# Kernel tuning notes

Measured on AMD Instinct MI355X. Metric: run time of the kernel, lower is better.

Reference implementation:

```python
import jax, jax.numpy as jnp
import numpy as np

N_NODES = 20000
N_EDGES = 500000
D_IN = 256
D_HID = 256
NUM_REL = 5
LL_OUT = 16
METAPATHS = [[0, 1], [2, 3]]  # relation id per hop, per metapath
N_CONVS = sum(len(mp) for mp in METAPATHS)  # 4 (all 256->256 since D_IN==D_HID)


def setup_inputs() -> dict:
    key = jax.random.key(0)
    ks = jax.random.split(key, 12)
    x = jax.random.normal(ks[0], (N_NODES, D_IN), dtype=jnp.float32)
    edge_index = jax.random.randint(ks[1], (2, N_EDGES), 0, N_NODES)
    edge_type = jax.random.randint(ks[2], (N_EDGES,), 0, NUM_REL)
    s = 1.0 / np.sqrt(D_HID)
    rel_W = jax.random.normal(ks[3], (N_CONVS, NUM_REL, D_HID, D_HID), dtype=jnp.float32) * s
    root_W = jax.random.normal(ks[4], (N_CONVS, D_HID, D_HID), dtype=jnp.float32) * s
    bias = jax.random.normal(ks[5], (N_CONVS, D_HID), dtype=jnp.float32) * s
    fc1_w = jax.random.normal(ks[6], (D_HID * len(METAPATHS), D_HID), dtype=jnp.float32) * s
    fc1_b = jnp.zeros((D_HID,), dtype=jnp.float32)
    fc2_w = jax.random.normal(ks[7], (D_HID, LL_OUT), dtype=jnp.float32) * s
    fc2_b = jnp.zeros((LL_OUT,), dtype=jnp.float32)
    return {"x": x, "edge_index": edge_index, "edge_type": edge_type,
            "rel_W": rel_W, "root_W": root_W, "bias": bias,
            "fc1_w": fc1_w, "fc1_b": fc1_b, "fc2_w": fc2_w, "fc2_b": fc2_b}


def _rgcn_conv(rel, h, W, R, b, src, dst, edge_type, n_nodes):
    # single-relation RGCN hop, flow='target_to_source': src node i aggregates
    # transformed features of its dst neighbors over edges with type==rel (mean).
    m = (edge_type == rel).astype(h.dtype)              # [E]
    hr = h @ W[rel]                                     # [N, D]
    msg = hr[dst] * m[:, None]                          # [E, D]
    agg = jax.ops.segment_sum(msg, src, num_segments=n_nodes)
    cnt = jax.ops.segment_sum(m, src, num_segments=n_nodes)
    agg = agg / jnp.maximum(cnt, 1.0)[:, None]
    return agg + h @ R + b


def reference(x, edge_index, edge_type, rel_W, root_W, bias, fc1_w, fc1_b, fc2_w, fc2_b):
    src, dst = edge_index[0], edge_index[1]
    n = x.shape[0]
    embs = []
    ci = 0
    for mp in METAPATHS:
        h = x
        for rel in mp:
            h = jax.nn.relu(_rgcn_conv(rel, h, rel_W[ci], root_W[ci], bias[ci],
                                       src, dst, edge_type, n))
            ci += 1
        embs.append(h)
    hcat = jnp.concatenate(embs, axis=1)                # [N, D_HID*n_metapaths]
    h = jax.nn.relu(hcat @ fc1_w + fc1_b)
    h = h @ fc2_w + fc2_b
    return jax.nn.log_softmax(h, axis=1)
```

## Files before the change

kernel.cpp:

```cpp
#include <hip/hip_runtime.h>
#include <hip/hip_bf16.h>

#define D 256
typedef unsigned short u16;
typedef __attribute__((ext_vector_type(8))) short bf16x8;
typedef __attribute__((ext_vector_type(4))) float f32x4;

__device__ inline u16 f2bf(float f) {
    unsigned u = __builtin_bit_cast(unsigned, f);
    unsigned r = (u + 0x7fff + ((u >> 16) & 1)) >> 16;
    return (u16)r;
}
__device__ inline float bf2f(u16 u) {
    return __builtin_bit_cast(float, (unsigned)u << 16);
}


__global__ void hist_kernel(const int* __restrict__ src, const int* __restrict__ et,
                            int* __restrict__ cnt, int E, int N) {
    int e = blockIdx.x * blockDim.x + threadIdx.x;
    if (e < E) {
        int r = et[e];
        if (r < 4) atomicAdd(&cnt[r * N + src[e]], 1);
    }
}

#define SCAN_BLK 4096

__global__ __launch_bounds__(256) void scan_reduce_kernel(const int* __restrict__ cnt,
        int* __restrict__ bsum, int n) {
    __shared__ int s[256];
    int base = blockIdx.x * SCAN_BLK;
    int t = threadIdx.x;
    int sum = 0;
    for (int i = t; i < SCAN_BLK; i += 256) {
        int idx = base + i;
        if (idx < n) sum += cnt[idx];
    }
    s[t] = sum;
    __syncthreads();
    for (int off = 128; off > 0; off >>= 1) {
        if (t < off) s[t] += s[t + off];
        __syncthreads();
    }
    if (t == 0) bsum[blockIdx.x] = s[0];
}

__global__ __launch_bounds__(256) void scan_sums_kernel(const int* __restrict__ bsum,
        int* __restrict__ boff, int nb, int* __restrict__ row_ptr, int n) {
    __shared__ int s[256];
    int t = threadIdx.x;
    s[t] = (t < nb) ? bsum[t] : 0;
    __syncthreads();
    for (int off = 1; off < 256; off <<= 1) {
        int v = (t >= off) ? s[t - off] : 0;
        __syncthreads();
        s[t] += v;
        __syncthreads();
    }
    if (t < nb) boff[t] = (t == 0) ? 0 : s[t - 1];
    if (t == 255) row_ptr[n] = s[255];
}

__global__ __launch_bounds__(256) void scan_out_kernel(const int* __restrict__ cnt,
        const int* __restrict__ boff, int* __restrict__ row_ptr,
        int* __restrict__ row_cur, int n) {
    __shared__ int stage[SCAN_BLK];
    __shared__ int part[256];
    int base = blockIdx.x * SCAN_BLK;
    int t = threadIdx.x;
    for (int i = t; i < SCAN_BLK; i += 256) {
        int idx = base + i;
        stage[i] = (idx < n) ? cnt[idx] : 0;
    }
    __syncthreads();
    int loc = 0;
#pragma unroll
    for (int j = 0; j < 16; ++j) loc += stage[t * 16 + j];
    part[t] = loc;
    __syncthreads();
    for (int off = 1; off < 256; off <<= 1) {
        int v = (t >= off) ? part[t - off] : 0;
        __syncthreads();
        part[t] += v;
        __syncthreads();
    }
    int run = boff[blockIdx.x] + ((t == 0) ? 0 : part[t - 1]);
#pragma unroll
    for (int j = 0; j < 16; ++j) {
        int idx = base + t * 16 + j;
        if (idx < n) {
            row_ptr[idx] = run;
            row_cur[idx] = run;
        }
        run += stage[t * 16 + j];
    }
}

__global__ void scatter_kernel(const int* __restrict__ src, const int* __restrict__ dst,
        const int* __restrict__ et, int* __restrict__ row_cur, int* __restrict__ eperm,
        int E, int N) {
    int e = blockIdx.x * blockDim.x + threadIdx.x;
    if (e < E) {
        int r = et[e];
        if (r < 4) {
            int pos = atomicAdd(&row_cur[r * N + src[e]], 1);
            eperm[pos] = dst[e];
        }
    }
}


__global__ void cast_x_kernel(const float* __restrict__ x, u16* __restrict__ xb, int n4) {
    int i = blockIdx.x * blockDim.x + threadIdx.x;
    if (i < n4) {
        float4 v = reinterpret_cast<const float4*>(x)[i];
        ushort4 o;
        o.x = f2bf(v.x); o.y = f2bf(v.y); o.z = f2bf(v.z); o.w = f2bf(v.w);
        reinterpret_cast<ushort4*>(xb)[i] = o;
    }
}

__global__ void build_wt_kernel(const float* __restrict__ rel_W,
                                const float* __restrict__ root_W, u16* __restrict__ Wcat) {
    int t = blockIdx.x * blockDim.x + threadIdx.x;
    int k = t & 255;
    int n = (t >> 8) & 511;
    int ci = t >> 17;
    float v;
    if (n < 256) v = rel_W[(((size_t)ci * 5 + ci) * 256 + k) * 256 + n];
    else         v = root_W[((size_t)ci * 256 + k) * 256 + (n - 256)];
    Wcat[t] = f2bf(v);
}

__global__ void build_fc1t_kernel(const float* __restrict__ fc1_w, u16* __restrict__ fc1t) {
    int t = blockIdx.x * blockDim.x + threadIdx.x;
    int k = t & 511;
    int n = t >> 9;
    fc1t[t] = f2bf(fc1_w[(size_t)k * 256 + n]);
}

__global__ void build_fc2t_kernel(const float* __restrict__ fc2_w, u16* __restrict__ fc2t) {
    int t = blockIdx.x * blockDim.x + threadIdx.x;
    int k = t & 255;
    int col = t >> 8;
    fc2t[t] = f2bf(fc2_w[(size_t)k * 16 + col]);
}


#define BM 64
#define BN 128
#define BK 64

template <int MODE>
__global__ __launch_bounds__(256) void gemm_mfma(
        const u16* __restrict__ A, const u16* __restrict__ Bt, int M, int K,
        u16* __restrict__ out_bf, u16* __restrict__ out_root,
        const float* __restrict__ bias, int ldo_bf) {
    __shared__ u16 Bs[BN * BK];

    const int tid  = threadIdx.x;
    const int wave = tid >> 6, lane = tid & 63;
    const int l15 = lane & 15, lg = lane >> 4;
    const int m0 = blockIdx.x * BM + wave * 16;
    const int n0 = blockIdx.y * BN;

    f32x4 acc[8];
#pragma unroll
    for (int j = 0; j < 8; ++j) acc[j] = (f32x4){0.f, 0.f, 0.f, 0.f};

    const int  arow = m0 + l15;
    const bool aval = arow < M;
    const u16* Arow = A + (size_t)arow * K;

    for (int k0 = 0; k0 < K; k0 += BK) {
        __syncthreads();
#pragma unroll
        for (int i = 0; i < 4; ++i) {
            int phys = i * 4096 + tid * 16;
            int n    = phys >> 7;
            int cl   = (phys & 127) ^ ((n & 7) << 4);
            const u16* srcp = Bt + (size_t)(n0 + n) * K + k0 + (cl >> 1);
            __builtin_amdgcn_global_load_lds(
                (const __attribute__((address_space(1))) void*)srcp,
                (__attribute__((address_space(3))) void*)((char*)Bs + phys), 16, 0, 0);
        }
        bf16x8 afr[2];
        if (aval) {
            afr[0] = *reinterpret_cast<const bf16x8*>(Arow + k0 + lg * 8);
            afr[1] = *reinterpret_cast<const bf16x8*>(Arow + k0 + 32 + lg * 8);
        } else {
            afr[0] = afr[1] = (bf16x8){0, 0, 0, 0, 0, 0, 0, 0};
        }
        __syncthreads();
#pragma unroll
        for (int kk = 0; kk < 2; ++kk) {
#pragma unroll
            for (int j = 0; j < 8; ++j) {
                int n    = j * 16 + l15;
                int cl   = kk * 64 + lg * 16;
                int phys = n * 128 + (cl ^ ((n & 7) << 4));
                bf16x8 bfr = *reinterpret_cast<const bf16x8*>((const char*)Bs + phys);
                acc[j] = __builtin_amdgcn_mfma_f32_16x16x32_bf16(afr[kk], bfr, acc[j], 0, 0, 0);
            }
        }
    }

    const int orow = m0 + lg * 4;
#pragma unroll
    for (int j = 0; j < 8; ++j) {
        int gn = n0 + j * 16 + l15;
#pragma unroll
        for (int r = 0; r < 4; ++r) {
            int m = orow + r;
            if (m >= M) continue;
            float v = acc[j][r];
            if (MODE == 0) {
                if (gn < 256) out_bf[(size_t)m * 256 + gn] = f2bf(v);
                else          out_root[(size_t)m * 256 + gn - 256] = f2bf(v + bias[gn - 256]);
            } else {
                v = fmaxf(v + bias[gn], 0.0f);
                out_bf[(size_t)m * ldo_bf + gn] = f2bf(v);
            }
        }
    }
}


__global__ __launch_bounds__(256) void aggregate_kernel(const u16* __restrict__ hr,
        const int* __restrict__ row_ptr, const int* __restrict__ eperm,
        const u16* __restrict__ rootb, u16* __restrict__ dst,
        int ldo, int coff, int N) {
    int node = blockIdx.x * 4 + (threadIdx.x >> 6);
    int lane = threadIdx.x & 63;
    if (node >= N) return;

    int beg = row_ptr[node];
    int end = row_ptr[node + 1];
    float a0 = 0.f, a1 = 0.f, a2 = 0.f, a3 = 0.f;
    for (int e = beg; e < end; ++e) {
        int d = eperm[e];
        ushort4 v = *reinterpret_cast<const ushort4*>(hr + (size_t)d * 256 + lane * 4);
        a0 += bf2f(v.x); a1 += bf2f(v.y); a2 += bf2f(v.z); a3 += bf2f(v.w);
    }
    float inv = 1.0f / fmaxf((float)(end - beg), 1.0f);
    ushort4 r4 = *reinterpret_cast<const ushort4*>(rootb + (size_t)node * 256 + lane * 4);
    ushort4 o;
    o.x = f2bf(fmaxf(fmaf(a0, inv, bf2f(r4.x)), 0.0f));
    o.y = f2bf(fmaxf(fmaf(a1, inv, bf2f(r4.y)), 0.0f));
    o.z = f2bf(fmaxf(fmaf(a2, inv, bf2f(r4.z)), 0.0f));
    o.w = f2bf(fmaxf(fmaf(a3, inv, bf2f(r4.w)), 0.0f));
    *reinterpret_cast<ushort4*>(dst + (size_t)node * ldo + coff + lane * 4) = o;
}


__global__ __launch_bounds__(256) void head_mfma_kernel(const u16* __restrict__ hid,
        const u16* __restrict__ w2t, const float* __restrict__ b2,
        float* __restrict__ out, int N) {
    int tile = blockIdx.x * 4 + (threadIdx.x >> 6);
    int lane = threadIdx.x & 63;
    int l15 = lane & 15, lg = lane >> 4;
    int ntiles = (N + 15) / 16;
    if (tile >= ntiles) return;

    int anode = tile * 16 + l15;
    if (anode >= N) anode = N - 1;
    const u16* Arow = hid + (size_t)anode * 256;
    const u16* Brow = w2t + (size_t)l15 * 256;

    f32x4 acc = (f32x4){0.f, 0.f, 0.f, 0.f};
#pragma unroll
    for (int k0 = 0; k0 < 256; k0 += 32) {
        bf16x8 a = *reinterpret_cast<const bf16x8*>(Arow + k0 + lg * 8);
        bf16x8 b = *reinterpret_cast<const bf16x8*>(Brow + k0 + lg * 8);
        acc = __builtin_amdgcn_mfma_f32_16x16x32_bf16(a, b, acc, 0, 0, 0);
    }
    float bcol = b2[l15];
#pragma unroll
    for (int r = 0; r < 4; ++r) {
        float v = acc[r] + bcol;
        float mx = v;
        mx = fmaxf(mx, __shfl_xor(mx, 1));
        mx = fmaxf(mx, __shfl_xor(mx, 2));
        mx = fmaxf(mx, __shfl_xor(mx, 4));
        mx = fmaxf(mx, __shfl_xor(mx, 8));
        float e = expf(v - mx);
        float s = e;
        s += __shfl_xor(s, 1);
        s += __shfl_xor(s, 2);
        s += __shfl_xor(s, 4);
        s += __shfl_xor(s, 8);
        float lse = mx + logf(s);
        int row = tile * 16 + lg * 4 + r;
        if (row < N) out[(size_t)row * 16 + l15] = v - lse;
    }
}


extern "C" void kernel_launch(void* const* d_in, const int* in_sizes, int n_in,
                              void* d_out, int out_size, void* d_ws, size_t ws_size,
                              hipStream_t stream) {
    const float* x      = (const float*)d_in[0];
    const int*   ei     = (const int*)d_in[1];
    const int*   et     = (const int*)d_in[2];
    const float* rel_W  = (const float*)d_in[3];
    const float* root_W = (const float*)d_in[4];
    const float* bias   = (const float*)d_in[5];
    const float* fc1_w  = (const float*)d_in[6];
    const float* fc1_b  = (const float*)d_in[7];
    const float* fc2_w  = (const float*)d_in[8];
    const float* fc2_b  = (const float*)d_in[9];
    float* out = (float*)d_out;

    const int N = in_sizes[0] / D;
    const int E = in_sizes[2];
    const int* src = ei;
    const int* dst = ei + E;

    char* w = (char*)d_ws;
    u16* xb    = (u16*)w;  w += (size_t)N * 256 * 2;
    u16* h1b   = (u16*)w;  w += (size_t)N * 256 * 2;
    u16* hcatb = (u16*)w;  w += (size_t)N * 512 * 2;
    u16* hr    = (u16*)w;  w += (size_t)N * 256 * 2;
    u16* rootb = (u16*)w;  w += (size_t)N * 256 * 2;
    u16* Wcat  = (u16*)w;  w += (size_t)4 * 512 * 256 * 2;
    u16* fc1t  = (u16*)w;  w += (size_t)256 * 512 * 2;
    u16* fc2t  = (u16*)w;  w += (size_t)16 * 256 * 2;
    int* cnt     = (int*)w;  w += (size_t)4 * N * 4;
    int* row_ptr = (int*)w;  w += ((size_t)4 * N + 1) * 4;
    int* row_cur = (int*)w;  w += (size_t)4 * N * 4;
    int* eperm   = (int*)w;  w += (size_t)E * 4;
    int* bsum    = (int*)w;  w += 256 * 4;
    int* boff    = (int*)w;  w += 256 * 4;
    u16* hid = h1b;

    const int n_keys = 4 * N;
    const int nb = (n_keys + SCAN_BLK - 1) / SCAN_BLK;

    hipMemsetAsync(cnt, 0, (size_t)n_keys * 4, stream);
    hist_kernel<<<dim3((E + 255) / 256), dim3(256), 0, stream>>>(src, et, cnt, E, N);
    scan_reduce_kernel<<<dim3(nb), dim3(256), 0, stream>>>(cnt, bsum, n_keys);
    scan_sums_kernel<<<dim3(1), dim3(256), 0, stream>>>(bsum, boff, nb, row_ptr, n_keys);
    scan_out_kernel<<<dim3(nb), dim3(256), 0, stream>>>(cnt, boff, row_ptr, row_cur, n_keys);
    scatter_kernel<<<dim3((E + 255) / 256), dim3(256), 0, stream>>>(src, dst, et, row_cur, eperm, E, N);

    cast_x_kernel<<<dim3((N * 256 / 4 + 255) / 256), dim3(256), 0, stream>>>(x, xb, N * 256 / 4);
    build_wt_kernel<<<dim3(4 * 512 * 256 / 256), dim3(256), 0, stream>>>(rel_W, root_W, Wcat);
    build_fc1t_kernel<<<dim3(256 * 512 / 256), dim3(256), 0, stream>>>(fc1_w, fc1t);
    build_fc2t_kernel<<<dim3(16), dim3(256), 0, stream>>>(fc2_w, fc2t);

    dim3 gblock(256);
    dim3 ngrid((N + 3) / 4);
    dim3 cgrid((N + BM - 1) / BM, 512 / BN);
    dim3 fgrid((N + BM - 1) / BM, 256 / BN);

    for (int ci = 0; ci < 4; ++ci) {
        int mp = ci >> 1, hop = ci & 1;
        const u16* hin = (hop == 0) ? xb : h1b;
        gemm_mfma<0><<<cgrid, gblock, 0, stream>>>(hin, Wcat + (size_t)ci * 512 * 256,
                N, 256, hr, rootb, bias + (size_t)ci * 256, 256);
        u16* dstb; int ldo, coff;
        if (hop == 0) { dstb = h1b;   ldo = 256; coff = 0; }
        else          { dstb = hcatb; ldo = 512; coff = mp * 256; }
        aggregate_kernel<<<ngrid, gblock, 0, stream>>>(hr, row_ptr + (size_t)ci * N, eperm,
                rootb, dstb, ldo, coff, N);
    }
    gemm_mfma<1><<<fgrid, gblock, 0, stream>>>(hcatb, fc1t, N, 512, hid, nullptr, fc1_b, 256);
    int ntiles = (N + 15) / 16;
    head_mfma_kernel<<<dim3((ntiles + 3) / 4), gblock, 0, stream>>>(hid, fc2t, fc2_b, out, N);
}
```

Measured before the change: 322.5 us.

## Aggregate before transform and fuse root GEMM via K-concatenated weights

Reorders each RGCN hop so neighbor features are mean-aggregated first and then multiplied by a stacked [W_rel; W_root] weight, making each hop one K=512 GEMM that reads [agg | h] and applies bias+ReLU in the epilogue. This removes the separate hr/rootb intermediates and the fused-output split. The first-hop aggregations of both metapaths share one launch over x. The four weight/cast prep kernels are merged into one prep kernel. The GEMM keeps the same FLOPs (K doubles, N halves), and aggregation now operates on input features instead of transformed ones.

```diff
diff --git a/kernel.cpp b/kernel.cpp
--- a/kernel.cpp
+++ b/kernel.cpp
@@ -111,59 +111,83 @@
 }
 
 
-__global__ void cast_x_kernel(const float* __restrict__ x, u16* __restrict__ xb, int n4) {
-    int i = blockIdx.x * blockDim.x + threadIdx.x;
-    if (i < n4) {
+__global__ __launch_bounds__(256) void prep_kernel(const float* __restrict__ x,
+        const float* __restrict__ rel_W, const float* __restrict__ root_W,
+        const float* __restrict__ fc1_w, const float* __restrict__ fc2_w,
+        u16* __restrict__ xb, u16* __restrict__ Bcat, u16* __restrict__ fc2t, int N) {
+    int i = blockIdx.x * 256 + threadIdx.x;
+    int nx = N * 64;
+    if (i < nx) {
         float4 v = reinterpret_cast<const float4*>(x)[i];
         ushort4 o;
         o.x = f2bf(v.x); o.y = f2bf(v.y); o.z = f2bf(v.z); o.w = f2bf(v.w);
         reinterpret_cast<ushort4*>(xb)[i] = o;
-    }
-}
-
-__global__ void build_wt_kernel(const float* __restrict__ rel_W,
-                                const float* __restrict__ root_W, u16* __restrict__ Wcat) {
-    int t = blockIdx.x * blockDim.x + threadIdx.x;
-    int k = t & 255;
-    int n = (t >> 8) & 511;
-    int ci = t >> 17;
-    float v;
-    if (n < 256) v = rel_W[(((size_t)ci * 5 + ci) * 256 + k) * 256 + n];
-    else         v = root_W[((size_t)ci * 256 + k) * 256 + (n - 256)];
-    Wcat[t] = f2bf(v);
-}
-
-__global__ void build_fc1t_kernel(const float* __restrict__ fc1_w, u16* __restrict__ fc1t) {
-    int t = blockIdx.x * blockDim.x + threadIdx.x;
-    int k = t & 511;
-    int n = t >> 9;
-    fc1t[t] = f2bf(fc1_w[(size_t)k * 256 + n]);
-}
-
-__global__ void build_fc2t_kernel(const float* __restrict__ fc2_w, u16* __restrict__ fc2t) {
-    int t = blockIdx.x * blockDim.x + threadIdx.x;
-    int k = t & 255;
-    int col = t >> 8;
-    fc2t[t] = f2bf(fc2_w[(size_t)k * 16 + col]);
-}
-
-
-#define BM 64
-#define BN 128
-#define BK 64
-
-template <int MODE>
-__global__ __launch_bounds__(256) void gemm_mfma(
-        const u16* __restrict__ A, const u16* __restrict__ Bt, int M, int K,
-        u16* __restrict__ out_bf, u16* __restrict__ out_root,
-        const float* __restrict__ bias, int ldo_bf) {
-    __shared__ u16 Bs[BN * BK];
+        return;
+    }
+    int j = i - nx;
+    if (j < 5 * 131072) {
+        int mi = j >> 17;
+        int t = j & 131071;
+        int k = t & 511;
+        int n = t >> 9;
+        float v;
+        if (mi < 4) {
+            v = (k < 256) ? rel_W[(((size_t)mi * 5 + mi) * 256 + k) * 256 + n]
+                          : root_W[((size_t)mi * 256 + (k - 256)) * 256 + n];
+        } else {
+            v = fc1_w[(size_t)k * 256 + n];
+        }
+        Bcat[(size_t)mi * 131072 + (size_t)n * 512 + k] = f2bf(v);
+        return;
+    }
+    int h = j - 5 * 131072;
+    if (h < 4096) {
+        int k = h & 255;
+        int col = h >> 8;
+        fc2t[(size_t)col * 256 + k] = f2bf(fc2_w[(size_t)k * 16 + col]);
+    }
+}
+
+
+__global__ __launch_bounds__(256) void agg_kernel(const u16* __restrict__ h,
+        const int* __restrict__ rpA, const int* __restrict__ rpB,
+        const int* __restrict__ eperm,
+        u16* __restrict__ outA, u16* __restrict__ outB, int N) {
+    int node = blockIdx.x * 4 + (threadIdx.x >> 6);
+    int lane = threadIdx.x & 63;
+    if (node >= N) return;
+    const int* rp = (blockIdx.y == 0) ? rpA : rpB;
+    u16* outp     = (blockIdx.y == 0) ? outA : outB;
+
+    int beg = rp[node];
+    int end = rp[node + 1];
+    float a0 = 0.f, a1 = 0.f, a2 = 0.f, a3 = 0.f;
+    for (int e = beg; e < end; ++e) {
+        int d = eperm[e];
+        ushort4 v = *reinterpret_cast<const ushort4*>(h + (size_t)d * 256 + lane * 4);
+        a0 += bf2f(v.x); a1 += bf2f(v.y); a2 += bf2f(v.z); a3 += bf2f(v.w);
+    }
+    float inv = 1.0f / fmaxf((float)(end - beg), 1.0f);
+    ushort4 o;
+    o.x = f2bf(a0 * inv);
+    o.y = f2bf(a1 * inv);
+    o.z = f2bf(a2 * inv);
+    o.w = f2bf(a3 * inv);
+    *reinterpret_cast<ushort4*>(outp + (size_t)node * 256 + lane * 4) = o;
+}
+
+
+__global__ __launch_bounds__(256) void gemm512(
+        const u16* __restrict__ Alo, int ldlo, const u16* __restrict__ Ahi, int ldhi,
+        const u16* __restrict__ Bt, int M,
+        u16* __restrict__ outp, int ldo, int coff, const float* __restrict__ bias) {
+    __shared__ u16 Bs[128 * 64];
 
     const int tid  = threadIdx.x;
     const int wave = tid >> 6, lane = tid & 63;
     const int l15 = lane & 15, lg = lane >> 4;
-    const int m0 = blockIdx.x * BM + wave * 16;
-    const int n0 = blockIdx.y * BN;
+    const int m0 = blockIdx.x * 64 + wave * 16;
+    const int n0 = blockIdx.y * 128;
 
     f32x4 acc[8];
 #pragma unroll
@@ -171,26 +195,28 @@
 
     const int  arow = m0 + l15;
     const bool aval = arow < M;
-    const u16* Arow = A + (size_t)arow * K;
-
-    for (int k0 = 0; k0 < K; k0 += BK) {
+
+#pragma unroll
+    for (int k0 = 0; k0 < 512; k0 += 64) {
         __syncthreads();
 #pragma unroll
         for (int i = 0; i < 4; ++i) {
             int phys = i * 4096 + tid * 16;
             int n    = phys >> 7;
             int cl   = (phys & 127) ^ ((n & 7) << 4);
-            const u16* srcp = Bt + (size_t)(n0 + n) * K + k0 + (cl >> 1);
+            const u16* srcp = Bt + (size_t)(n0 + n) * 512 + k0 + (cl >> 1);
             __builtin_amdgcn_global_load_lds(
                 (const __attribute__((address_space(1))) void*)srcp,
                 (__attribute__((address_space(3))) void*)((char*)Bs + phys), 16, 0, 0);
         }
-        bf16x8 afr[2];
+        const u16* Ab = (k0 < 256) ? (Alo + (size_t)arow * ldlo + k0)
+                                   : (Ahi + (size_t)arow * ldhi + (k0 - 256));
+        bf16x8 afr0, afr1;
         if (aval) {
-            afr[0] = *reinterpret_cast<const bf16x8*>(Arow + k0 + lg * 8);
-            afr[1] = *reinterpret_cast<const bf16x8*>(Arow + k0 + 32 + lg * 8);
+            afr0 = *reinterpret_cast<const bf16x8*>(Ab + lg * 8);
+            afr1 = *reinterpret_cast<const bf16x8*>(Ab + 32 + lg * 8);
         } else {
-            afr[0] = afr[1] = (bf16x8){0, 0, 0, 0, 0, 0, 0, 0};
+            afr0 = afr1 = (bf16x8){0, 0, 0, 0, 0, 0, 0, 0};
         }
         __syncthreads();
 #pragma unroll
@@ -201,7 +227,7 @@
                 int cl   = kk * 64 + lg * 16;
                 int phys = n * 128 + (cl ^ ((n & 7) << 4));
                 bf16x8 bfr = *reinterpret_cast<const bf16x8*>((const char*)Bs + phys);
-                acc[j] = __builtin_amdgcn_mfma_f32_16x16x32_bf16(afr[kk], bfr, acc[j], 0, 0, 0);
+                acc[j] = __builtin_amdgcn_mfma_f32_16x16x32_bf16(kk ? afr1 : afr0, bfr, acc[j], 0, 0, 0);
             }
         }
     }
@@ -210,47 +236,15 @@
 #pragma unroll
     for (int j = 0; j < 8; ++j) {
         int gn = n0 + j * 16 + l15;
+        float b = bias[gn];
 #pragma unroll
         for (int r = 0; r < 4; ++r) {
             int m = orow + r;
             if (m >= M) continue;
-            float v = acc[j][r];
-            if (MODE == 0) {
-                if (gn < 256) out_bf[(size_t)m * 256 + gn] = f2bf(v);
-                else          out_root[(size_t)m * 256 + gn - 256] = f2bf(v + bias[gn - 256]);
-            } else {
-                v = fmaxf(v + bias[gn], 0.0f);
-                out_bf[(size_t)m * ldo_bf + gn] = f2bf(v);
-            }
-        }
-    }
-}
-
-
-__global__ __launch_bounds__(256) void aggregate_kernel(const u16* __restrict__ hr,
-        const int* __restrict__ row_ptr, const int* __restrict__ eperm,
-        const u16* __restrict__ rootb, u16* __restrict__ dst,
-        int ldo, int coff, int N) {
-    int node = blockIdx.x * 4 + (threadIdx.x >> 6);
-    int lane = threadIdx.x & 63;
-    if (node >= N) return;
-
-    int beg = row_ptr[node];
-    int end = row_ptr[node + 1];
-    float a0 = 0.f, a1 = 0.f, a2 = 0.f, a3 = 0.f;
-    for (int e = beg; e < end; ++e) {
-        int d = eperm[e];
-        ushort4 v = *reinterpret_cast<const ushort4*>(hr + (size_t)d * 256 + lane * 4);
-        a0 += bf2f(v.x); a1 += bf2f(v.y); a2 += bf2f(v.z); a3 += bf2f(v.w);
-    }
-    float inv = 1.0f / fmaxf((float)(end - beg), 1.0f);
-    ushort4 r4 = *reinterpret_cast<const ushort4*>(rootb + (size_t)node * 256 + lane * 4);
-    ushort4 o;
-    o.x = f2bf(fmaxf(fmaf(a0, inv, bf2f(r4.x)), 0.0f));
-    o.y = f2bf(fmaxf(fmaf(a1, inv, bf2f(r4.y)), 0.0f));
-    o.z = f2bf(fmaxf(fmaf(a2, inv, bf2f(r4.z)), 0.0f));
-    o.w = f2bf(fmaxf(fmaf(a3, inv, bf2f(r4.w)), 0.0f));
-    *reinterpret_cast<ushort4*>(dst + (size_t)node * ldo + coff + lane * 4) = o;
+            float v = fmaxf(acc[j][r] + b, 0.0f);
+            outp[(size_t)m * ldo + coff + gn] = f2bf(v);
+        }
+    }
 }
 
 
@@ -321,10 +315,9 @@
     u16* xb    = (u16*)w;  w += (size_t)N * 256 * 2;
     u16* h1b   = (u16*)w;  w += (size_t)N * 256 * 2;
     u16* hcatb = (u16*)w;  w += (size_t)N * 512 * 2;
-    u16* hr    = (u16*)w;  w += (size_t)N * 256 * 2;
-    u16* rootb = (u16*)w;  w += (size_t)N * 256 * 2;
-    u16* Wcat  = (u16*)w;  w += (size_t)4 * 512 * 256 * 2;
-    u16* fc1t  = (u16*)w;  w += (size_t)256 * 512 * 2;
+    u16* aggA  = (u16*)w;  w += (size_t)N * 256 * 2;
+    u16* aggB  = (u16*)w;  w += (size_t)N * 256 * 2;
+    u16* Bcat  = (u16*)w;  w += (size_t)5 * 256 * 512 * 2;
     u16* fc2t  = (u16*)w;  w += (size_t)16 * 256 * 2;
     int* cnt     = (int*)w;  w += (size_t)4 * N * 4;
     int* row_ptr = (int*)w;  w += ((size_t)4 * N + 1) * 4;
@@ -344,28 +337,31 @@
     scan_out_kernel<<<dim3(nb), dim3(256), 0, stream>>>(cnt, boff, row_ptr, row_cur, n_keys);
     scatter_kernel<<<dim3((E + 255) / 256), dim3(256), 0, stream>>>(src, dst, et, row_cur, eperm, E, N);
 
-    cast_x_kernel<<<dim3((N * 256 / 4 + 255) / 256), dim3(256), 0, stream>>>(x, xb, N * 256 / 4);
-    build_wt_kernel<<<dim3(4 * 512 * 256 / 256), dim3(256), 0, stream>>>(rel_W, root_W, Wcat);
-    build_fc1t_kernel<<<dim3(256 * 512 / 256), dim3(256), 0, stream>>>(fc1_w, fc1t);
-    build_fc2t_kernel<<<dim3(16), dim3(256), 0, stream>>>(fc2_w, fc2t);
+    {
+        int total = N * 64 + 5 * 131072 + 4096;
+        prep_kernel<<<dim3((total + 255) / 256), dim3(256), 0, stream>>>(
+                x, rel_W, root_W, fc1_w, fc2_w, xb, Bcat, fc2t, N);
+    }
 
     dim3 gblock(256);
-    dim3 ngrid((N + 3) / 4);
-    dim3 cgrid((N + BM - 1) / BM, 512 / BN);
-    dim3 fgrid((N + BM - 1) / BM, 256 / BN);
-
-    for (int ci = 0; ci < 4; ++ci) {
-        int mp = ci >> 1, hop = ci & 1;
-        const u16* hin = (hop == 0) ? xb : h1b;
-        gemm_mfma<0><<<cgrid, gblock, 0, stream>>>(hin, Wcat + (size_t)ci * 512 * 256,
-                N, 256, hr, rootb, bias + (size_t)ci * 256, 256);
-        u16* dstb; int ldo, coff;
-        if (hop == 0) { dstb = h1b;   ldo = 256; coff = 0; }
-        else          { dstb = hcatb; ldo = 512; coff = mp * 256; }
-        aggregate_kernel<<<ngrid, gblock, 0, stream>>>(hr, row_ptr + (size_t)ci * N, eperm,
-                rootb, dstb, ldo, coff, N);
-    }
-    gemm_mfma<1><<<fgrid, gblock, 0, stream>>>(hcatb, fc1t, N, 512, hid, nullptr, fc1_b, 256);
+    dim3 ngrid1((N + 3) / 4, 1);
+    dim3 ngrid2((N + 3) / 4, 2);
+    dim3 ggrid((N + 63) / 64, 2);
+
+    agg_kernel<<<ngrid2, gblock, 0, stream>>>(xb, row_ptr, row_ptr + 2 * N, eperm, aggA, aggB, N);
+
+    gemm512<<<ggrid, gblock, 0, stream>>>(aggA, 256, xb, 256, Bcat + 0 * 131072, N,
+                                          h1b, 256, 0, bias + 0 * 256);
+    agg_kernel<<<ngrid1, gblock, 0, stream>>>(h1b, row_ptr + 1 * N, row_ptr + 1 * N, eperm, aggA, aggA, N);
+    gemm512<<<ggrid, gblock, 0, stream>>>(aggA, 256, h1b, 256, Bcat + 1 * 131072, N,
+                                          hcatb, 512, 0, bias + 1 * 256);
+    gemm512<<<ggrid, gblock, 0, stream>>>(aggB, 256, xb, 256, Bcat + 2 * 131072, N,
+                                          h1b, 256, 0, bias + 2 * 256);
+    agg_kernel<<<ngrid1, gblock, 0, stream>>>(h1b, row_ptr + 3 * N, row_ptr + 3 * N, eperm, aggA, aggA, N);
+    gemm512<<<ggrid, gblock, 0, stream>>>(aggA, 256, h1b, 256, Bcat + 3 * 131072, N,
+                                          hcatb, 512, 256, bias + 3 * 256);
+    gemm512<<<ggrid, gblock, 0, stream>>>(hcatb, 512, hcatb + 256, 512, Bcat + 4 * 131072, N,
+                                          hid, 256, 0, fc1_b);
     int ntiles = (N + 15) / 16;
     head_mfma_kernel<<<dim3((ntiles + 3) / 4), gblock, 0, stream>>>(hid, fc2t, fc2_b, out, N);
 }
```

Result: faster. 301.2 us (-6.6%).
